# Performance work log

Measured on AMD Instinct MI355X. Metric: run time of the kernel, lower is better.

## Reference

```python
import jax, jax.numpy as jnp
import numpy as np


def setup_inputs() -> dict:
    key = jax.random.key(0)
    k1, k2, k3, k4 = jax.random.split(key, 4)
    B, H, S, D = 2, 16, 2048, 64
    q = jax.random.normal(k1, (B, H, S, D), dtype=jnp.float32)
    k = jax.random.normal(k2, (B, H, S, D), dtype=jnp.float32)
    v = jax.random.normal(k3, (B, H, S, D), dtype=jnp.float32)
    mask = jax.random.randint(k4, (1, 1, S, S), 0, 2, dtype=jnp.int32)
    return {"q": q, "k": k, "v": v, "mask": mask}


def reference(q, k, v, mask):
    # scores: [B,H,S,S] -- intentionally materialized as in the original
    d = k.shape[-1]
    scale = 1.0 / jnp.sqrt(jnp.asarray(d, dtype=q.dtype))
    x = jnp.einsum("bhqd,bhkd->bhqk", q, k) * scale
    x = x + mask.astype(x.dtype) * jnp.asarray(-10000.0, dtype=x.dtype)
    p = jax.nn.softmax(x, axis=-1)  # dropout is identity in eval mode
    return jnp.einsum("bhqk,bhkd->bhqd", p, v)
```

## Files before the change

### kernel.cpp

```cpp
#include <hip/hip_runtime.h>


#define S_LEN 2048
#define D_DIM 64
#define N_KT 32
#define LDK 72
#define LDV 72
#define TILE_SHORTS (64 * 72)
#define TILE_BYTES (TILE_SHORTS * 2)
#define NBH 32

typedef __attribute__((ext_vector_type(8))) short bf16x8;
typedef __attribute__((ext_vector_type(16))) float f32x16;
typedef unsigned int u32;
typedef unsigned long long u64;

#define C1 0.180336880111121f
#define CM (-14426.9504088896f)

static __device__ __forceinline__ unsigned short f2bf(float f) {
  union { float f; unsigned u; } x; x.f = f;
  return (unsigned short)((x.u + 0x8000u) >> 16);
}
static __device__ __forceinline__ unsigned packbf(float lo, float hi) {
  union { float f; unsigned u; } a, b; a.f = lo; b.f = hi;
  return ((a.u + 0x8000u) >> 16) | ((b.u + 0x8000u) & 0xffff0000u);
}
static __device__ __forceinline__ f32x16 zero16() {
  f32x16 z;
#pragma unroll
  for (int i = 0; i < 16; ++i) z[i] = 0.f;
  return z;
}
static __device__ __forceinline__ void dma16(const u32* g, u32* l) {
  __builtin_amdgcn_global_load_lds(
      (const __attribute__((address_space(1))) u32*)g,
      (__attribute__((address_space(3))) u32*)l, 16, 0, 0);
}

__global__ __launch_bounds__(256) void prep_kv(
    const float* __restrict__ k, const float* __restrict__ v,
    unsigned short* __restrict__ kws, unsigned short* __restrict__ vws) {
  const int kt = blockIdx.x, bh = blockIdx.y;
  const int t = threadIdx.x;
  __shared__ unsigned short Vt[TILE_SHORTS];
  const size_t goff = (size_t)bh * (S_LEN * D_DIM) + (size_t)kt * 64 * D_DIM;
  const float4* kg = (const float4*)(k + goff);
  const float4* vg = (const float4*)(v + goff);
  unsigned short* kimg = kws + (size_t)(bh * N_KT + kt) * TILE_SHORTS;
#pragma unroll
  for (int j = 0; j < 4; ++j) {
    const int i = t + j * 256;
    const int row = i >> 4, c4 = i & 15;
    const float4 x = kg[i];
    ushort4 w;
    w.x = f2bf(x.x); w.y = f2bf(x.y); w.z = f2bf(x.z); w.w = f2bf(x.w);
    *(ushort4*)&kimg[row * LDK + c4 * 4] = w;
    const float4 y = vg[i];
    const int swc = 8 * (((row >> 3) + c4) & 7) + (row & 7);
    Vt[(4 * c4 + 0) * LDV + swc] = f2bf(y.x);
    Vt[(4 * c4 + 1) * LDV + swc] = f2bf(y.y);
    Vt[(4 * c4 + 2) * LDV + swc] = f2bf(y.z);
    Vt[(4 * c4 + 3) * LDV + swc] = f2bf(y.w);
  }
  __syncthreads();
  uint4* vimg = (uint4*)(vws + (size_t)(bh * N_KT + kt) * TILE_SHORTS);
  const uint4* lv = (const uint4*)Vt;
  for (int i = t; i < TILE_BYTES / 16; i += 256) vimg[i] = lv[i];
}

__global__ __launch_bounds__(256) void prep_mask(
    const int* __restrict__ mask, u64* __restrict__ mb) {
  const int pair = blockIdx.x * 4 + (threadIdx.x >> 6);
  const int lane = threadIdx.x & 63;
  const int row = pair >> 5, kt = pair & 31;
  const int mv = mask[(size_t)row * S_LEN + kt * 64 + lane];
  const u64 b = __ballot(mv != 0);
  if (lane == 0) mb[pair] = b;
}

__global__ __launch_bounds__(128, 2) void attn_fwd(
    const float* __restrict__ q, const unsigned short* __restrict__ kws,
    const unsigned short* __restrict__ vws, const u64* __restrict__ mb,
    float* __restrict__ out) {
  const int qt = blockIdx.x;
  const int bh = blockIdx.y;
  const size_t hoff = (size_t)bh * (S_LEN * D_DIM);

  __shared__ unsigned short Ks[2][TILE_SHORTS];
  __shared__ unsigned short Vt[2][TILE_SHORTS];

  const int t = threadIdx.x;
  const int wave = t >> 6;
  const int lane = t & 63;
  const int col = lane & 31;
  const int hl = lane >> 5;
  const int sw = col >> 2;

  const int qg = qt * 64 + wave * 32 + col;

  bf16x8 bQ[4];
  {
    const float* qrow = q + hoff + (size_t)qg * D_DIM;
#pragma unroll
    for (int ks = 0; ks < 4; ++ks) {
      const float4 x0 = *(const float4*)(qrow + ks * 16 + hl * 8);
      const float4 x1 = *(const float4*)(qrow + ks * 16 + hl * 8 + 4);
      union { bf16x8 v; unsigned d[4]; } u;
      u.d[0] = packbf(x0.x, x0.y);
      u.d[1] = packbf(x0.z, x0.w);
      u.d[2] = packbf(x1.x, x1.y);
      u.d[3] = packbf(x1.z, x1.w);
      bQ[ks] = u.v;
    }
  }

  const unsigned short* kbase = kws + (size_t)bh * N_KT * TILE_SHORTS;
  const unsigned short* vbase = vws + (size_t)bh * N_KT * TILE_SHORTS;

  f32x16 oT0 = zero16(), oT1 = zero16();
  float lacc = 0.f;
  const u64* mrow = mb + (size_t)qg * N_KT;

  {
    const u32* g = (const u32*)((wave == 0 ? kbase : vbase));
    u32* l = wave == 0 ? (u32*)&Ks[0][0] : (u32*)&Vt[0][0];
#pragma unroll
    for (int i = 0; i < 9; ++i) dma16(g + i * 256 + lane * 4, l + i * 256);
  }

  for (int kt = 0; kt < N_KT; ++kt) {
    __syncthreads();
    if (kt + 1 < N_KT) {
      const u32* g = (const u32*)((wave == 0 ? kbase : vbase) +
                                  (size_t)(kt + 1) * TILE_SHORTS);
      u32* l = wave == 0 ? (u32*)&Ks[(kt + 1) & 1][0]
                         : (u32*)&Vt[(kt + 1) & 1][0];
#pragma unroll
      for (int i = 0; i < 9; ++i) dma16(g + i * 256 + lane * 4, l + i * 256);
    }
    const u64 mw = mrow[kt];
    const unsigned short* Ksb = Ks[kt & 1];
    const unsigned short* Vtb = Vt[kt & 1];

    f32x16 sT0 = zero16(), sT1 = zero16();
#pragma unroll
    for (int ks = 0; ks < 4; ++ks) {
      const bf16x8 aK0 = *(const bf16x8*)&Ksb[col * LDK + ks * 16 + hl * 8];
      const bf16x8 aK1 = *(const bf16x8*)&Ksb[(32 + col) * LDK + ks * 16 + hl * 8];
      sT0 = __builtin_amdgcn_mfma_f32_32x32x16_bf16(aK0, bQ[ks], sT0, 0, 0, 0);
      sT1 = __builtin_amdgcn_mfma_f32_32x32x16_bf16(aK1, bQ[ks], sT1, 0, 0, 0);
    }

    unsigned pw[2][8];
#pragma unroll
    for (int kb = 0; kb < 2; ++kb) {
      const unsigned w = kb ? (unsigned)(mw >> 32) : (unsigned)mw;
      const f32x16 sT = kb ? sT1 : sT0;
      float e[16];
#pragma unroll
      for (int g = 0; g < 4; ++g) {
        const unsigned nib = (w >> (8 * g + 4 * hl)) & 0xFu;
#pragma unroll
        for (int r3 = 0; r3 < 4; ++r3) {
          const int reg = g * 4 + r3;
          const float bias = (nib & (1u << r3)) ? CM : 0.0f;
          const float ev = __builtin_amdgcn_exp2f(fmaf(sT[reg], C1, bias));
          e[reg] = ev;
          lacc += ev;
        }
        pw[kb][g * 2 + 0] = packbf(e[g * 4 + 0], e[g * 4 + 1]);
        pw[kb][g * 2 + 1] = packbf(e[g * 4 + 2], e[g * 4 + 3]);
      }
    }

#pragma unroll
    for (int ks = 0; ks < 4; ++ks) {
      const int kb = ks >> 1, h = ks & 1;
      const unsigned d0 = pw[kb][4 * h + 0], d1 = pw[kb][4 * h + 1];
      const unsigned d2 = pw[kb][4 * h + 2], d3 = pw[kb][4 * h + 3];
      const unsigned s0 = hl ? d0 : d2;
      const unsigned s1 = hl ? d1 : d3;
      const unsigned r0 = (unsigned)__shfl_xor((int)s0, 32);
      const unsigned r1 = (unsigned)__shfl_xor((int)s1, 32);
      union { bf16x8 v; unsigned d[4]; } pf;
      pf.d[0] = hl ? r0 : d0;
      pf.d[1] = hl ? r1 : d1;
      pf.d[2] = hl ? d2 : r0;
      pf.d[3] = hl ? d3 : r1;
      const int cpr = 8 * (((2 * ks + hl) + sw) & 7);
      const bf16x8 aV0 = *(const bf16x8*)&Vtb[col * LDV + cpr];
      const bf16x8 aV1 = *(const bf16x8*)&Vtb[(32 + col) * LDV + cpr];
      oT0 = __builtin_amdgcn_mfma_f32_32x32x16_bf16(aV0, pf.v, oT0, 0, 0, 0);
      oT1 = __builtin_amdgcn_mfma_f32_32x32x16_bf16(aV1, pf.v, oT1, 0, 0, 0);
    }
  }

  const float ltot = lacc + __shfl_xor(lacc, 32);
  const float inv = 1.0f / ltot;
  float* orow = out + hoff + (size_t)qg * D_DIM;
#pragma unroll
  for (int rg = 0; rg < 4; ++rg) {
    float4 w0, w1;
    w0.x = oT0[rg * 4 + 0] * inv; w0.y = oT0[rg * 4 + 1] * inv;
    w0.z = oT0[rg * 4 + 2] * inv; w0.w = oT0[rg * 4 + 3] * inv;
    w1.x = oT1[rg * 4 + 0] * inv; w1.y = oT1[rg * 4 + 1] * inv;
    w1.z = oT1[rg * 4 + 2] * inv; w1.w = oT1[rg * 4 + 3] * inv;
    *(float4*)(orow + 8 * rg + 4 * hl) = w0;
    *(float4*)(orow + 32 + 8 * rg + 4 * hl) = w1;
  }
}

__global__ __launch_bounds__(256, 2) void attn_fwd_self(
    const float* __restrict__ q, const float* __restrict__ k,
    const float* __restrict__ v, const int* __restrict__ mask,
    float* __restrict__ out) {
  const int qt = blockIdx.x;
  const int bh = blockIdx.y;
  const size_t hoff = (size_t)bh * (S_LEN * D_DIM);
  __shared__ unsigned short Ks[64 * LDK];
  __shared__ unsigned short Vt[64 * LDV];
  const int t = threadIdx.x;
  const int wave = t >> 6;
  const int lane = t & 63;
  const int col = lane & 31;
  const int hl = lane >> 5;
  const int sw = col >> 2;
  const int qg = qt * 128 + wave * 32 + col;
  bf16x8 bQ[4];
  {
    const float* qrow = q + hoff + (size_t)qg * D_DIM;
#pragma unroll
    for (int ks = 0; ks < 4; ++ks) {
      const float4 x0 = *(const float4*)(qrow + ks * 16 + hl * 8);
      const float4 x1 = *(const float4*)(qrow + ks * 16 + hl * 8 + 4);
      union { bf16x8 v; unsigned d[4]; } u;
      u.d[0] = packbf(x0.x, x0.y);
      u.d[1] = packbf(x0.z, x0.w);
      u.d[2] = packbf(x1.x, x1.y);
      u.d[3] = packbf(x1.z, x1.w);
      bQ[ks] = u.v;
    }
  }
  float4 pk[4], pv[4];
  {
    const float4* kg = (const float4*)(k + hoff);
    const float4* vg = (const float4*)(v + hoff);
#pragma unroll
    for (int j = 0; j < 4; ++j) { pk[j] = kg[t + j * 256]; pv[j] = vg[t + j * 256]; }
  }
  f32x16 oT0 = zero16(), oT1 = zero16();
  float lacc = 0.f;
  const int* mrow = mask + (size_t)qg * S_LEN;
  for (int kt = 0; kt < N_KT; ++kt) {
    __syncthreads();
#pragma unroll
    for (int j = 0; j < 4; ++j) {
      const int i = t + j * 256;
      const int row = i >> 4, c4 = i & 15;
      ushort4 w;
      w.x = f2bf(pk[j].x); w.y = f2bf(pk[j].y);
      w.z = f2bf(pk[j].z); w.w = f2bf(pk[j].w);
      *(ushort4*)&Ks[row * LDK + c4 * 4] = w;
      const int swc = 8 * (((row >> 3) + c4) & 7) + (row & 7);
      Vt[(4 * c4 + 0) * LDV + swc] = f2bf(pv[j].x);
      Vt[(4 * c4 + 1) * LDV + swc] = f2bf(pv[j].y);
      Vt[(4 * c4 + 2) * LDV + swc] = f2bf(pv[j].z);
      Vt[(4 * c4 + 3) * LDV + swc] = f2bf(pv[j].w);
    }
    __syncthreads();
    if (kt + 1 < N_KT) {
      const float4* kg = (const float4*)(k + hoff + (size_t)(kt + 1) * 64 * D_DIM);
      const float4* vg = (const float4*)(v + hoff + (size_t)(kt + 1) * 64 * D_DIM);
#pragma unroll
      for (int j = 0; j < 4; ++j) { pk[j] = kg[t + j * 256]; pv[j] = vg[t + j * 256]; }
    }
    int4 mq[2][4];
#pragma unroll
    for (int kb = 0; kb < 2; ++kb)
#pragma unroll
      for (int g = 0; g < 4; ++g)
        mq[kb][g] = *(const int4*)(mrow + kt * 64 + kb * 32 + g * 8 + hl * 4);
    f32x16 sT0 = zero16(), sT1 = zero16();
#pragma unroll
    for (int ks = 0; ks < 4; ++ks) {
      const bf16x8 aK0 = *(const bf16x8*)&Ks[col * LDK + ks * 16 + hl * 8];
      const bf16x8 aK1 = *(const bf16x8*)&Ks[(32 + col) * LDK + ks * 16 + hl * 8];
      sT0 = __builtin_amdgcn_mfma_f32_32x32x16_bf16(aK0, bQ[ks], sT0, 0, 0, 0);
      sT1 = __builtin_amdgcn_mfma_f32_32x32x16_bf16(aK1, bQ[ks], sT1, 0, 0, 0);
    }
    unsigned pw[2][8];
#pragma unroll
    for (int kb = 0; kb < 2; ++kb) {
      const f32x16 sT = kb ? sT1 : sT0;
      float e[16];
#pragma unroll
      for (int g = 0; g < 4; ++g) {
        const int4 mv = mq[kb][g];
        const int* mvp = &mv.x;
#pragma unroll
        for (int r3 = 0; r3 < 4; ++r3) {
          const int reg = g * 4 + r3;
          const float bias = mvp[r3] ? CM : 0.0f;
          const float ev = __builtin_amdgcn_exp2f(fmaf(sT[reg], C1, bias));
          e[reg] = ev;
          lacc += ev;
        }
        pw[kb][g * 2 + 0] = packbf(e[g * 4 + 0], e[g * 4 + 1]);
        pw[kb][g * 2 + 1] = packbf(e[g * 4 + 2], e[g * 4 + 3]);
      }
    }
#pragma unroll
    for (int ks = 0; ks < 4; ++ks) {
      const int kb = ks >> 1, h = ks & 1;
      const unsigned d0 = pw[kb][4 * h + 0], d1 = pw[kb][4 * h + 1];
      const unsigned d2 = pw[kb][4 * h + 2], d3 = pw[kb][4 * h + 3];
      const unsigned s0 = hl ? d0 : d2;
      const unsigned s1 = hl ? d1 : d3;
      const unsigned r0 = (unsigned)__shfl_xor((int)s0, 32);
      const unsigned r1 = (unsigned)__shfl_xor((int)s1, 32);
      union { bf16x8 v; unsigned d[4]; } pf;
      pf.d[0] = hl ? r0 : d0;
      pf.d[1] = hl ? r1 : d1;
      pf.d[2] = hl ? d2 : r0;
      pf.d[3] = hl ? d3 : r1;
      const int cpr = 8 * (((2 * ks + hl) + sw) & 7);
      const bf16x8 aV0 = *(const bf16x8*)&Vt[col * LDV + cpr];
      const bf16x8 aV1 = *(const bf16x8*)&Vt[(32 + col) * LDV + cpr];
      oT0 = __builtin_amdgcn_mfma_f32_32x32x16_bf16(aV0, pf.v, oT0, 0, 0, 0);
      oT1 = __builtin_amdgcn_mfma_f32_32x32x16_bf16(aV1, pf.v, oT1, 0, 0, 0);
    }
  }
  const float ltot = lacc + __shfl_xor(lacc, 32);
  const float inv = 1.0f / ltot;
  float* orow = out + hoff + (size_t)qg * D_DIM;
#pragma unroll
  for (int rg = 0; rg < 4; ++rg) {
    float4 w0, w1;
    w0.x = oT0[rg * 4 + 0] * inv; w0.y = oT0[rg * 4 + 1] * inv;
    w0.z = oT0[rg * 4 + 2] * inv; w0.w = oT0[rg * 4 + 3] * inv;
    w1.x = oT1[rg * 4 + 0] * inv; w1.y = oT1[rg * 4 + 1] * inv;
    w1.z = oT1[rg * 4 + 2] * inv; w1.w = oT1[rg * 4 + 3] * inv;
    *(float4*)(orow + 8 * rg + 4 * hl) = w0;
    *(float4*)(orow + 32 + 8 * rg + 4 * hl) = w1;
  }
}

extern "C" void kernel_launch(void* const* d_in, const int* in_sizes, int n_in,
                              void* d_out, int out_size, void* d_ws, size_t ws_size,
                              hipStream_t stream) {
  const float* q = (const float*)d_in[0];
  const float* k = (const float*)d_in[1];
  const float* v = (const float*)d_in[2];
  const int* mask = (const int*)d_in[3];
  float* out = (float*)d_out;

  const size_t img_elems = (size_t)NBH * N_KT * TILE_SHORTS;
  const size_t mb_words = (size_t)S_LEN * N_KT;
  const size_t need = img_elems * 2 * sizeof(unsigned short) + mb_words * 8;

  if (ws_size >= need) {
    unsigned short* kws = (unsigned short*)d_ws;
    unsigned short* vws = kws + img_elems;
    u64* mbp = (u64*)(vws + img_elems);
    prep_kv<<<dim3(N_KT, NBH), dim3(256), 0, stream>>>(k, v, kws, vws);
    prep_mask<<<dim3((S_LEN * N_KT) / 4), dim3(256), 0, stream>>>(mask, mbp);
    attn_fwd<<<dim3(S_LEN / 64, NBH), dim3(128), 0, stream>>>(q, kws, vws, mbp, out);
  } else {
    attn_fwd_self<<<dim3(S_LEN / 128, NBH), dim3(256), 0, stream>>>(q, k, v, mask, out);
  }
}
```

Measured before the change: 174.0 us.

## Precompute fp16 mask words, fold scale into Q, compute row sums with MFMA

The softmax scale is folded into Q when it is converted to bf16, so each score feeds exp2 directly. The mask is preprocessed into per-lane fp16-pair AND masks that zero masked probabilities instead of adding a large negative bias before exp. P and V move to fp16 and use the f16 MFMA. The row-sum accumulation is replaced by an extra MFMA against a ones vector. The aim is to cut per-element VALU work in the softmax. In exchange the mask workspace grows considerably, each lane loads more mask data per tile, and each step adds one MFMA.

```diff
diff --git a/kernel.cpp b/kernel.cpp
--- a/kernel.cpp
+++ b/kernel.cpp
@@ -12,6 +12,7 @@
 
 typedef __attribute__((ext_vector_type(8))) short bf16x8;
 typedef __attribute__((ext_vector_type(16))) float f32x16;
+typedef __attribute__((ext_vector_type(2))) __fp16 fp16x2;
 typedef unsigned int u32;
 typedef unsigned long long u64;
 
@@ -36,6 +37,11 @@
   __builtin_amdgcn_global_load_lds(
       (const __attribute__((address_space(1))) u32*)g,
       (__attribute__((address_space(3))) u32*)l, 16, 0, 0);
+}
+static __device__ __forceinline__ unsigned pkh(float lo, float hi) {
+  union { fp16x2 h; unsigned u; } x;
+  x.h = __builtin_amdgcn_cvt_pkrtz(lo, hi);
+  return x.u;
 }
 
 __global__ __launch_bounds__(256) void prep_kv(
@@ -58,10 +64,12 @@
     *(ushort4*)&kimg[row * LDK + c4 * 4] = w;
     const float4 y = vg[i];
     const int swc = 8 * (((row >> 3) + c4) & 7) + (row & 7);
-    Vt[(4 * c4 + 0) * LDV + swc] = f2bf(y.x);
-    Vt[(4 * c4 + 1) * LDV + swc] = f2bf(y.y);
-    Vt[(4 * c4 + 2) * LDV + swc] = f2bf(y.z);
-    Vt[(4 * c4 + 3) * LDV + swc] = f2bf(y.w);
+    const unsigned p01 = pkh(y.x, y.y);
+    const unsigned p23 = pkh(y.z, y.w);
+    Vt[(4 * c4 + 0) * LDV + swc] = (unsigned short)(p01 & 0xffff);
+    Vt[(4 * c4 + 1) * LDV + swc] = (unsigned short)(p01 >> 16);
+    Vt[(4 * c4 + 2) * LDV + swc] = (unsigned short)(p23 & 0xffff);
+    Vt[(4 * c4 + 3) * LDV + swc] = (unsigned short)(p23 >> 16);
   }
   __syncthreads();
   uint4* vimg = (uint4*)(vws + (size_t)(bh * N_KT + kt) * TILE_SHORTS);
@@ -70,18 +78,26 @@
 }
 
 __global__ __launch_bounds__(256) void prep_mask(
-    const int* __restrict__ mask, u64* __restrict__ mb) {
-  const int pair = blockIdx.x * 4 + (threadIdx.x >> 6);
+    const int* __restrict__ mask, u32* __restrict__ mw) {
+  const int wid = blockIdx.x * 4 + (threadIdx.x >> 6);
   const int lane = threadIdx.x & 63;
-  const int row = pair >> 5, kt = pair & 31;
+  const int row = wid >> 5, kt = wid & 31;
   const int mv = mask[(size_t)row * S_LEN + kt * 64 + lane];
   const u64 b = __ballot(mv != 0);
-  if (lane == 0) mb[pair] = b;
+  if (lane < 32) {
+    const int hl = lane >> 4, p = lane & 15;
+    const int kb = p >> 3, g = (p >> 1) & 3, h = p & 1;
+    const int j0 = 32 * kb + 8 * g + 4 * hl + 2 * h;
+    u32 w = 0;
+    if (!((b >> j0) & 1)) w |= 0x0000FFFFu;
+    if (!((b >> (j0 + 1)) & 1)) w |= 0xFFFF0000u;
+    mw[((size_t)(row * 2 + hl) * N_KT + kt) * 16 + p] = w;
+  }
 }
 
 __global__ __launch_bounds__(128, 2) void attn_fwd(
     const float* __restrict__ q, const unsigned short* __restrict__ kws,
-    const unsigned short* __restrict__ vws, const u64* __restrict__ mb,
+    const unsigned short* __restrict__ vws, const u32* __restrict__ mw,
     float* __restrict__ out) {
   const int qt = blockIdx.x;
   const int bh = blockIdx.y;
@@ -107,20 +123,26 @@
       const float4 x0 = *(const float4*)(qrow + ks * 16 + hl * 8);
       const float4 x1 = *(const float4*)(qrow + ks * 16 + hl * 8 + 4);
       union { bf16x8 v; unsigned d[4]; } u;
-      u.d[0] = packbf(x0.x, x0.y);
-      u.d[1] = packbf(x0.z, x0.w);
-      u.d[2] = packbf(x1.x, x1.y);
-      u.d[3] = packbf(x1.z, x1.w);
+      u.d[0] = packbf(x0.x * C1, x0.y * C1);
+      u.d[1] = packbf(x0.z * C1, x0.w * C1);
+      u.d[2] = packbf(x1.x * C1, x1.y * C1);
+      u.d[3] = packbf(x1.z * C1, x1.w * C1);
       bQ[ks] = u.v;
     }
+  }
+
+  bf16x8 onesA;
+  {
+    union { bf16x8 v; unsigned d[4]; } u;
+    u.d[0] = u.d[1] = u.d[2] = u.d[3] = 0x3C003C00u;
+    onesA = u.v;
   }
 
   const unsigned short* kbase = kws + (size_t)bh * N_KT * TILE_SHORTS;
   const unsigned short* vbase = vws + (size_t)bh * N_KT * TILE_SHORTS;
 
-  f32x16 oT0 = zero16(), oT1 = zero16();
-  float lacc = 0.f;
-  const u64* mrow = mb + (size_t)qg * N_KT;
+  f32x16 oT0 = zero16(), oT1 = zero16(), oL = zero16();
+  const uint4* mrow = (const uint4*)(mw + (size_t)(qg * 2 + hl) * N_KT * 16);
 
   {
     const u32* g = (const u32*)((wave == 0 ? kbase : vbase));
@@ -139,7 +161,10 @@
 #pragma unroll
       for (int i = 0; i < 9; ++i) dma16(g + i * 256 + lane * 4, l + i * 256);
     }
-    const u64 mw = mrow[kt];
+    uint4 mq0 = mrow[kt * 4 + 0], mq1 = mrow[kt * 4 + 1];
+    uint4 mq2 = mrow[kt * 4 + 2], mq3 = mrow[kt * 4 + 3];
+    const u32 mwv[16] = {mq0.x, mq0.y, mq0.z, mq0.w, mq1.x, mq1.y, mq1.z, mq1.w,
+                         mq2.x, mq2.y, mq2.z, mq2.w, mq3.x, mq3.y, mq3.z, mq3.w};
     const unsigned short* Ksb = Ks[kt & 1];
     const unsigned short* Vtb = Vt[kt & 1];
 
@@ -152,33 +177,26 @@
       sT1 = __builtin_amdgcn_mfma_f32_32x32x16_bf16(aK1, bQ[ks], sT1, 0, 0, 0);
     }
 
-    unsigned pw[2][8];
+    unsigned pw[16];
 #pragma unroll
     for (int kb = 0; kb < 2; ++kb) {
-      const unsigned w = kb ? (unsigned)(mw >> 32) : (unsigned)mw;
       const f32x16 sT = kb ? sT1 : sT0;
-      float e[16];
 #pragma unroll
       for (int g = 0; g < 4; ++g) {
-        const unsigned nib = (w >> (8 * g + 4 * hl)) & 0xFu;
-#pragma unroll
-        for (int r3 = 0; r3 < 4; ++r3) {
-          const int reg = g * 4 + r3;
-          const float bias = (nib & (1u << r3)) ? CM : 0.0f;
-          const float ev = __builtin_amdgcn_exp2f(fmaf(sT[reg], C1, bias));
-          e[reg] = ev;
-          lacc += ev;
-        }
-        pw[kb][g * 2 + 0] = packbf(e[g * 4 + 0], e[g * 4 + 1]);
-        pw[kb][g * 2 + 1] = packbf(e[g * 4 + 2], e[g * 4 + 3]);
+        const float e0 = __builtin_amdgcn_exp2f(sT[g * 4 + 0]);
+        const float e1 = __builtin_amdgcn_exp2f(sT[g * 4 + 1]);
+        const float e2 = __builtin_amdgcn_exp2f(sT[g * 4 + 2]);
+        const float e3 = __builtin_amdgcn_exp2f(sT[g * 4 + 3]);
+        pw[kb * 8 + g * 2 + 0] = pkh(e0, e1) & mwv[kb * 8 + g * 2 + 0];
+        pw[kb * 8 + g * 2 + 1] = pkh(e2, e3) & mwv[kb * 8 + g * 2 + 1];
       }
     }
 
 #pragma unroll
     for (int ks = 0; ks < 4; ++ks) {
       const int kb = ks >> 1, h = ks & 1;
-      const unsigned d0 = pw[kb][4 * h + 0], d1 = pw[kb][4 * h + 1];
-      const unsigned d2 = pw[kb][4 * h + 2], d3 = pw[kb][4 * h + 3];
+      const unsigned d0 = pw[kb * 8 + 4 * h + 0], d1 = pw[kb * 8 + 4 * h + 1];
+      const unsigned d2 = pw[kb * 8 + 4 * h + 2], d3 = pw[kb * 8 + 4 * h + 3];
       const unsigned s0 = hl ? d0 : d2;
       const unsigned s1 = hl ? d1 : d3;
       const unsigned r0 = (unsigned)__shfl_xor((int)s0, 32);
@@ -191,13 +209,13 @@
       const int cpr = 8 * (((2 * ks + hl) + sw) & 7);
       const bf16x8 aV0 = *(const bf16x8*)&Vtb[col * LDV + cpr];
       const bf16x8 aV1 = *(const bf16x8*)&Vtb[(32 + col) * LDV + cpr];
-      oT0 = __builtin_amdgcn_mfma_f32_32x32x16_bf16(aV0, pf.v, oT0, 0, 0, 0);
-      oT1 = __builtin_amdgcn_mfma_f32_32x32x16_bf16(aV1, pf.v, oT1, 0, 0, 0);
-    }
-  }
-
-  const float ltot = lacc + __shfl_xor(lacc, 32);
-  const float inv = 1.0f / ltot;
+      oT0 = __builtin_amdgcn_mfma_f32_32x32x16_f16(aV0, pf.v, oT0, 0, 0, 0);
+      oT1 = __builtin_amdgcn_mfma_f32_32x32x16_f16(aV1, pf.v, oT1, 0, 0, 0);
+      oL = __builtin_amdgcn_mfma_f32_32x32x16_f16(onesA, pf.v, oL, 0, 0, 0);
+    }
+  }
+
+  const float inv = 1.0f / oL[0];
   float* orow = out + hoff + (size_t)qg * D_DIM;
 #pragma unroll
   for (int rg = 0; rg < 4; ++rg) {
@@ -356,16 +374,16 @@
   float* out = (float*)d_out;
 
   const size_t img_elems = (size_t)NBH * N_KT * TILE_SHORTS;
-  const size_t mb_words = (size_t)S_LEN * N_KT;
-  const size_t need = img_elems * 2 * sizeof(unsigned short) + mb_words * 8;
+  const size_t mw_words = (size_t)S_LEN * 2 * N_KT * 16;
+  const size_t need = img_elems * 2 * sizeof(unsigned short) + mw_words * 4;
 
   if (ws_size >= need) {
     unsigned short* kws = (unsigned short*)d_ws;
     unsigned short* vws = kws + img_elems;
-    u64* mbp = (u64*)(vws + img_elems);
+    u32* mwp = (u32*)(vws + img_elems);
     prep_kv<<<dim3(N_KT, NBH), dim3(256), 0, stream>>>(k, v, kws, vws);
-    prep_mask<<<dim3((S_LEN * N_KT) / 4), dim3(256), 0, stream>>>(mask, mbp);
-    attn_fwd<<<dim3(S_LEN / 64, NBH), dim3(128), 0, stream>>>(q, kws, vws, mbp, out);
+    prep_mask<<<dim3((S_LEN * N_KT) / 4), dim3(256), 0, stream>>>(mask, mwp);
+    attn_fwd<<<dim3(S_LEN / 64, NBH), dim3(128), 0, stream>>>(q, kws, vws, mwp, out);
   } else {
     attn_fwd_self<<<dim3(S_LEN / 128, NBH), dim3(256), 0, stream>>>(q, k, v, mask, out);
   }
```

Measured after the change: 169.8 us. 2.4% less time.
